# Performance work log

Measured on AMD Instinct MI355X. Metric: run time of the kernel, lower is better.

## Reference

```python
import jax, jax.numpy as jnp
import numpy as np

T, N = 64, 128          # temporal / spatial graph sizes; M = T*N product-graph nodes
B, F_IN, HID, F_OUT = 2, 32, 32, 16
L, K = 2, 4             # num_layers, filter order


def _sym_norm(key, n):
    # random symmetric adjacency, then D^{-1/2} A D^{-1/2} / 2 as in the torch __init__
    a = jax.random.uniform(key, (n, n), dtype=jnp.float32)
    a = 0.5 * (a + a.T)
    d = jnp.sum(a, axis=1)
    dinv = 1.0 / jnp.sqrt(d)
    return (dinv[:, None] * a * dinv[None, :]) * 0.5


def setup_inputs() -> dict:
    key = jax.random.key(0)
    ks = jax.random.split(key, 9)
    x = jax.random.normal(ks[0], (B, T * N, F_IN), dtype=jnp.float32)
    Adj_t = _sym_norm(ks[1], T)
    Adj_s = _sym_norm(ks[2], N)
    s = jax.random.normal(ks[3], (4,), dtype=jnp.float32) * 0.25
    H = jax.random.normal(ks[4], (L, K, HID, HID), dtype=jnp.float32) * 0.1
    W1 = jax.random.normal(ks[5], (F_IN, HID), dtype=jnp.float32) * (1.0 / np.sqrt(F_IN))
    b1 = jax.random.normal(ks[6], (HID,), dtype=jnp.float32) * 0.01
    W2 = jax.random.normal(ks[7], (HID, F_OUT), dtype=jnp.float32) * (1.0 / np.sqrt(HID))
    b2 = jax.random.normal(ks[8], (F_OUT,), dtype=jnp.float32) * 0.01
    return {"x": x, "Adj_t": Adj_t, "Adj_s": Adj_s, "s": s, "H": H,
            "W1": W1, "b1": b1, "W2": W2, "b2": b2}


def reference(x, Adj_t, Adj_s, s, H, W1, b1, W2, b2):
    t, n = Adj_t.shape[0], Adj_s.shape[0]
    I_t = jnp.eye(t, dtype=jnp.float32)
    I_s = jnp.eye(n, dtype=jnp.float32)
    # Adj = s0*I + s1*kron(I_t, Adj_s) + s2*kron(Adj_t, I_s) + s3*kron(Adj_t, Adj_s)
    Adj = (s[0] * jnp.eye(t * n, dtype=jnp.float32)
           + s[1] * jnp.kron(I_t, Adj_s)
           + s[2] * jnp.kron(Adj_t, I_s)
           + s[3] * jnp.kron(Adj_t, Adj_s))
    h = x @ W1 + b1                                   # [B, M, HID]
    num_layers = H.shape[0]
    for l in range(num_layers):
        Ah = jnp.einsum('mn,bnh->bmh', Adj, h)        # Adj @ x, hoisted out of k-loop
        # sum_k (Adj@x) @ H[l,k]  ==  einsum over k and h simultaneously
        h = jnp.tanh(jnp.einsum('bmh,khf->bmf', Ah, H[l]))
    return h @ W2 + b2                                # [B, M, F_OUT]
```

## Files before the change

kernel.cpp:

```cpp
#include <hip/hip_runtime.h>

#define T_DIM 64
#define N_DIM 128
#define BATCH 2
#define HIDW  32


__device__ __forceinline__ int rfl(int x) { return __builtin_amdgcn_readfirstlane(x); }

template<bool PROJ>
__global__ __launch_bounds__(512) void k_temporal(
    const float* __restrict__ src,
    const float* __restrict__ At,
    const float* __restrict__ W1, const float* __restrict__ b1,
    const float* __restrict__ s,
    const float* __restrict__ H, float* __restrict__ Hsum_ws,
    float* __restrict__ up, float* __restrict__ pp)
{
    __shared__ float At_s[64 * 68];
    __shared__ float xs[64 * 36];
    __shared__ float h_loc[64 * 36];

    const int tid = threadIdx.x;
    const int b   = blockIdx.x >> 7;
    const int n   = blockIdx.x & 127;
    const int fg  = tid >> 6;
    const int t   = tid & 63;
    const int fg4u = rfl(fg * 4);

    const float s0v = s[0], s1v = s[1], s2v = s[2], s3v = s[3];

    if (PROJ && blockIdx.x < 4) {
        int idx = blockIdx.x * 512 + tid;
        int l = idx >> 10, rem = idx & 1023;
        const float* Hl = H + l * 4096;
        Hsum_ws[idx] = Hl[rem] + Hl[1024 + rem] + Hl[2048 + rem] + Hl[3072 + rem];
    }

#pragma unroll
    for (int i = 0; i < 8; ++i) {
        int p = tid + 512 * i;
        At_s[(p >> 6) * 68 + (p & 63)] = At[p];
    }

    float h0, h1, h2, h3;
    if (PROJ) {
        {
            int tt = tid >> 3, c4 = tid & 7;
            float4 v = *(const float4*)(src + ((size_t)(b * 8192 + tt * 128 + n)) * 32 + c4 * 4);
            *(float4*)&xs[tt * 36 + c4 * 4] = v;
        }
        __syncthreads();
        const float* W1u = W1 + fg4u;
        float4 bv = *(const float4*)(b1 + fg4u);
        h0 = bv.x; h1 = bv.y; h2 = bv.z; h3 = bv.w;
#pragma unroll
        for (int k4 = 0; k4 < 8; ++k4) {
            float4 xv = *(const float4*)&xs[t * 36 + k4 * 4];
            float4 w0 = *(const float4*)(W1u + (k4 * 4 + 0) * 32);
            float4 w1 = *(const float4*)(W1u + (k4 * 4 + 1) * 32);
            float4 w2 = *(const float4*)(W1u + (k4 * 4 + 2) * 32);
            float4 w3 = *(const float4*)(W1u + (k4 * 4 + 3) * 32);
            h0 += xv.x * w0.x + xv.y * w1.x + xv.z * w2.x + xv.w * w3.x;
            h1 += xv.x * w0.y + xv.y * w1.y + xv.z * w2.y + xv.w * w3.y;
            h2 += xv.x * w0.z + xv.y * w1.z + xv.z * w2.z + xv.w * w3.z;
            h3 += xv.x * w0.w + xv.y * w1.w + xv.z * w2.w + xv.w * w3.w;
        }
        float4 hv; hv.x = h0; hv.y = h1; hv.z = h2; hv.w = h3;
        *(float4*)&h_loc[t * 36 + fg * 4] = hv;
        __syncthreads();
    } else {
        __syncthreads();
        float4 hv = *(const float4*)(src + (((size_t)(b * 128 + n)) * 64 + t) * 32 + fg * 4);
        h0 = hv.x; h1 = hv.y; h2 = hv.z; h3 = hv.w;
    }

    float w0 = 0.f, w1 = 0.f, w2 = 0.f, w3 = 0.f;
    const float* hrow = PROJ ? nullptr
                             : (src + rfl((b * 128 + n) * 2048) + fg4u);
#pragma unroll
    for (int u4 = 0; u4 < 16; ++u4) {
        float4 av = *(const float4*)&At_s[t * 68 + u4 * 4];
        float4 g0, g1, g2, g3;
        if (PROJ) {
            g0 = *(const float4*)&h_loc[(u4 * 4 + 0) * 36 + fg * 4];
            g1 = *(const float4*)&h_loc[(u4 * 4 + 1) * 36 + fg * 4];
            g2 = *(const float4*)&h_loc[(u4 * 4 + 2) * 36 + fg * 4];
            g3 = *(const float4*)&h_loc[(u4 * 4 + 3) * 36 + fg * 4];
        } else {
            g0 = *(const float4*)(hrow + (u4 * 4 + 0) * 32);
            g1 = *(const float4*)(hrow + (u4 * 4 + 1) * 32);
            g2 = *(const float4*)(hrow + (u4 * 4 + 2) * 32);
            g3 = *(const float4*)(hrow + (u4 * 4 + 3) * 32);
        }
        w0 += av.x * g0.x + av.y * g1.x + av.z * g2.x + av.w * g3.x;
        w1 += av.x * g0.y + av.y * g1.y + av.z * g2.y + av.w * g3.y;
        w2 += av.x * g0.z + av.y * g1.z + av.z * g2.z + av.w * g3.z;
        w3 += av.x * g0.w + av.y * g1.w + av.z * g2.w + av.w * g3.w;
    }
    float4 u4v, p4v;
    u4v.x = s1v * h0 + s3v * w0;  p4v.x = s0v * h0 + s2v * w0;
    u4v.y = s1v * h1 + s3v * w1;  p4v.y = s0v * h1 + s2v * w1;
    u4v.z = s1v * h2 + s3v * w2;  p4v.z = s0v * h2 + s2v * w2;
    u4v.w = s1v * h3 + s3v * w3;  p4v.w = s0v * h3 + s2v * w3;
    size_t base = ((size_t)((b * 64 + t) * 128 + n)) * 32 + fg * 4;
    *(float4*)(up + base) = u4v;
    *(float4*)(pp + base) = p4v;
}

template<bool LAST>
__global__ __launch_bounds__(512) void k_spatial(
    const float* __restrict__ up, const float* __restrict__ pp,
    const float* __restrict__ As, const float* __restrict__ Hsum_ws, int layer,
    const float* __restrict__ W2, const float* __restrict__ b2,
    float* __restrict__ hout, float* __restrict__ out)
{
    __shared__ float As_s[64 * 132];
    __shared__ float Ah_s[64 * 36];
    __shared__ float T_s[64 * 36];

    const int tid = threadIdx.x;
    const int b   = blockIdx.x >> 7;
    const int t   = (blockIdx.x >> 1) & 63;
    const int mh  = blockIdx.x & 1;
    const int fg  = tid >> 6;
    const int m   = tid & 63;
    const int fg4u = rfl(fg * 4);

#pragma unroll
    for (int i = 0; i < 4; ++i) {
        int p = tid + 512 * i;
        int r = p >> 5, g = p & 31;
        float4 v = *(const float4*)(As + ((size_t)(mh * 64 + r)) * 128 + g * 4);
        *(float4*)&As_s[r * 132 + g * 4] = v;
    }
    float4 pv = *(const float4*)(pp + (((size_t)(b * 64 + t)) * 128 + mh * 64 + m) * 32 + fg * 4);
    float a0 = pv.x, a1 = pv.y, a2 = pv.z, a3 = pv.w;
    __syncthreads();

    const float* urow = up + rfl((b * 64 + t) * 4096) + fg4u;
#pragma unroll 8
    for (int n4 = 0; n4 < 32; ++n4) {
        float4 av = *(const float4*)&As_s[m * 132 + n4 * 4];
        float4 u0 = *(const float4*)(urow + (n4 * 4 + 0) * 32);
        float4 u1 = *(const float4*)(urow + (n4 * 4 + 1) * 32);
        float4 u2 = *(const float4*)(urow + (n4 * 4 + 2) * 32);
        float4 u3 = *(const float4*)(urow + (n4 * 4 + 3) * 32);
        a0 += av.x * u0.x + av.y * u1.x + av.z * u2.x + av.w * u3.x;
        a1 += av.x * u0.y + av.y * u1.y + av.z * u2.y + av.w * u3.y;
        a2 += av.x * u0.z + av.y * u1.z + av.z * u2.z + av.w * u3.z;
        a3 += av.x * u0.w + av.y * u1.w + av.z * u2.w + av.w * u3.w;
    }
    {
        float4 w; w.x = a0; w.y = a1; w.z = a2; w.w = a3;
        *(float4*)&Ah_s[m * 36 + fg * 4] = w;
    }
    __syncthreads();

    const float* hsrow = Hsum_ws + rfl(layer * 1024) + fg4u;
    float c0 = 0.f, c1 = 0.f, c2 = 0.f, c3 = 0.f;
#pragma unroll
    for (int k4 = 0; k4 < 8; ++k4) {
        float4 av = *(const float4*)&Ah_s[m * 36 + k4 * 4];
        float4 q0 = *(const float4*)(hsrow + (k4 * 4 + 0) * 32);
        float4 q1 = *(const float4*)(hsrow + (k4 * 4 + 1) * 32);
        float4 q2 = *(const float4*)(hsrow + (k4 * 4 + 2) * 32);
        float4 q3 = *(const float4*)(hsrow + (k4 * 4 + 3) * 32);
        c0 += av.x * q0.x + av.y * q1.x + av.z * q2.x + av.w * q3.x;
        c1 += av.x * q0.y + av.y * q1.y + av.z * q2.y + av.w * q3.y;
        c2 += av.x * q0.z + av.y * q1.z + av.z * q2.z + av.w * q3.z;
        c3 += av.x * q0.w + av.y * q1.w + av.z * q2.w + av.w * q3.w;
    }
    c0 = tanhf(c0); c1 = tanhf(c1); c2 = tanhf(c2); c3 = tanhf(c3);

    if (!LAST) {
        float4 o; o.x = c0; o.y = c1; o.z = c2; o.w = c3;
        *(float4*)(hout + (((size_t)(b * 128 + mh * 64 + m)) * 64 + t) * 32 + fg * 4) = o;
    } else {
        float4 w; w.x = c0; w.y = c1; w.z = c2; w.w = c3;
        *(float4*)&T_s[m * 36 + fg * 4] = w;
        __syncthreads();
        const int fg2u = rfl(fg * 2);
        float o0 = b2[fg2u], o1 = b2[fg2u + 1];
        const float* w2r = W2 + fg2u;
#pragma unroll
        for (int k4 = 0; k4 < 8; ++k4) {
            float4 tv = *(const float4*)&T_s[m * 36 + k4 * 4];
            float2 v0 = *(const float2*)(w2r + (k4 * 4 + 0) * 16);
            float2 v1 = *(const float2*)(w2r + (k4 * 4 + 1) * 16);
            float2 v2 = *(const float2*)(w2r + (k4 * 4 + 2) * 16);
            float2 v3 = *(const float2*)(w2r + (k4 * 4 + 3) * 16);
            o0 += tv.x * v0.x + tv.y * v1.x + tv.z * v2.x + tv.w * v3.x;
            o1 += tv.x * v0.y + tv.y * v1.y + tv.z * v2.y + tv.w * v3.y;
        }
        float2 o; o.x = o0; o.y = o1;
        *(float2*)(out + (((size_t)(b * 64 + t)) * 128 + mh * 64 + m) * 16 + fg * 2) = o;
    }
}

extern "C" void kernel_launch(void* const* d_in, const int* in_sizes, int n_in,
                              void* d_out, int out_size, void* d_ws, size_t ws_size,
                              hipStream_t stream)
{
    const float* x   = (const float*)d_in[0];
    const float* At  = (const float*)d_in[1];
    const float* As  = (const float*)d_in[2];
    const float* s   = (const float*)d_in[3];
    const float* H   = (const float*)d_in[4];
    const float* W1  = (const float*)d_in[5];
    const float* b1  = (const float*)d_in[6];
    const float* W2  = (const float*)d_in[7];
    const float* b2  = (const float*)d_in[8];
    float* out = (float*)d_out;

    float* up   = (float*)d_ws;
    float* pp   = up + 524288;
    float* h    = pp + 524288;
    float* Hsum = h  + 524288;

    k_temporal<true ><<<256, 512, 0, stream>>>(x, At, W1, b1, s, H, Hsum, up, pp);
    k_spatial <false><<<256, 512, 0, stream>>>(up, pp, As, Hsum, 0, W2, b2, h, out);
    k_temporal<false><<<256, 512, 0, stream>>>(h, At, W1, b1, s, H, Hsum, up, pp);
    k_spatial <true ><<<256, 512, 0, stream>>>(up, pp, As, Hsum, 1, W2, b2, h, out);
}
```

Baseline: 40.13 us.

## Stage operands in XOR-swizzled shared memory and compute H sums per block

Replaces padded shared-memory layouts with an XOR swizzle and stages more operands in LDS. W1, W2, the spatial up-row and the temporal h-tile now go to shared memory instead of being read from global memory inside the inner loops. The per-layer sum of H over k is now computed redundantly in every spatial block rather than in a few blocks of the first kernel, which removes the Hsum workspace. The intent is cheaper, conflict-free LDS reads in place of repeated global loads, at the cost of higher LDS use per block (which may lower occupancy) and duplicated H summation.

```diff
diff --git a/kernel.cpp b/kernel.cpp
--- a/kernel.cpp
+++ b/kernel.cpp
@@ -1,12 +1,7 @@
 #include <hip/hip_runtime.h>
 
-#define T_DIM 64
-#define N_DIM 128
-#define BATCH 2
-#define HIDW  32
-
-
-__device__ __forceinline__ int rfl(int x) { return __builtin_amdgcn_readfirstlane(x); }
+
+__device__ __forceinline__ int swz(int row, int g) { return g ^ (row & 7); }
 
 template<bool PROJ>
 __global__ __launch_bounds__(512) void k_temporal(
@@ -14,110 +9,99 @@
     const float* __restrict__ At,
     const float* __restrict__ W1, const float* __restrict__ b1,
     const float* __restrict__ s,
-    const float* __restrict__ H, float* __restrict__ Hsum_ws,
     float* __restrict__ up, float* __restrict__ pp)
 {
-    __shared__ float At_s[64 * 68];
-    __shared__ float xs[64 * 36];
-    __shared__ float h_loc[64 * 36];
+    __shared__ float At_s[64 * 64];
+    __shared__ float xs  [64 * 32];
+    __shared__ float hls [64 * 32];
+    __shared__ float W1s [1024];
 
     const int tid = threadIdx.x;
     const int b   = blockIdx.x >> 7;
     const int n   = blockIdx.x & 127;
     const int fg  = tid >> 6;
-    const int t   = tid & 63;
-    const int fg4u = rfl(fg * 4);
+    const int lt  = tid & 63;
 
     const float s0v = s[0], s1v = s[1], s2v = s[2], s3v = s[3];
-
-    if (PROJ && blockIdx.x < 4) {
-        int idx = blockIdx.x * 512 + tid;
-        int l = idx >> 10, rem = idx & 1023;
-        const float* Hl = H + l * 4096;
-        Hsum_ws[idx] = Hl[rem] + Hl[1024 + rem] + Hl[2048 + rem] + Hl[3072 + rem];
-    }
 
 #pragma unroll
     for (int i = 0; i < 8; ++i) {
         int p = tid + 512 * i;
-        At_s[(p >> 6) * 68 + (p & 63)] = At[p];
-    }
-
-    float h0, h1, h2, h3;
+        int r = p >> 6, c = p & 63;
+        At_s[r * 64 + (swz(r, c >> 2) << 2) + (c & 3)] = At[p];
+    }
+
     if (PROJ) {
         {
             int tt = tid >> 3, c4 = tid & 7;
             float4 v = *(const float4*)(src + ((size_t)(b * 8192 + tt * 128 + n)) * 32 + c4 * 4);
-            *(float4*)&xs[tt * 36 + c4 * 4] = v;
-        }
-        __syncthreads();
-        const float* W1u = W1 + fg4u;
-        float4 bv = *(const float4*)(b1 + fg4u);
-        h0 = bv.x; h1 = bv.y; h2 = bv.z; h3 = bv.w;
+            *(float4*)&xs[tt * 32 + (swz(tt, c4) << 2)] = v;
+        }
+        if (tid < 256) ((float4*)W1s)[tid] = ((const float4*)W1)[tid];
+        __syncthreads();
+        float4 bv = *(const float4*)(b1 + fg * 4);
+        float h0 = bv.x, h1 = bv.y, h2 = bv.z, h3 = bv.w;
 #pragma unroll
         for (int k4 = 0; k4 < 8; ++k4) {
-            float4 xv = *(const float4*)&xs[t * 36 + k4 * 4];
-            float4 w0 = *(const float4*)(W1u + (k4 * 4 + 0) * 32);
-            float4 w1 = *(const float4*)(W1u + (k4 * 4 + 1) * 32);
-            float4 w2 = *(const float4*)(W1u + (k4 * 4 + 2) * 32);
-            float4 w3 = *(const float4*)(W1u + (k4 * 4 + 3) * 32);
+            float4 xv = *(const float4*)&xs[lt * 32 + (swz(lt, k4) << 2)];
+            float4 w0 = *(const float4*)&W1s[(k4 * 4 + 0) * 32 + fg * 4];
+            float4 w1 = *(const float4*)&W1s[(k4 * 4 + 1) * 32 + fg * 4];
+            float4 w2 = *(const float4*)&W1s[(k4 * 4 + 2) * 32 + fg * 4];
+            float4 w3 = *(const float4*)&W1s[(k4 * 4 + 3) * 32 + fg * 4];
             h0 += xv.x * w0.x + xv.y * w1.x + xv.z * w2.x + xv.w * w3.x;
             h1 += xv.x * w0.y + xv.y * w1.y + xv.z * w2.y + xv.w * w3.y;
             h2 += xv.x * w0.z + xv.y * w1.z + xv.z * w2.z + xv.w * w3.z;
             h3 += xv.x * w0.w + xv.y * w1.w + xv.z * w2.w + xv.w * w3.w;
         }
         float4 hv; hv.x = h0; hv.y = h1; hv.z = h2; hv.w = h3;
-        *(float4*)&h_loc[t * 36 + fg * 4] = hv;
+        *(float4*)&hls[lt * 32 + (swz(lt, fg) << 2)] = hv;
         __syncthreads();
     } else {
-        __syncthreads();
-        float4 hv = *(const float4*)(src + (((size_t)(b * 128 + n)) * 64 + t) * 32 + fg * 4);
-        h0 = hv.x; h1 = hv.y; h2 = hv.z; h3 = hv.w;
-    }
-
+        {
+            int tt = tid >> 3, c4 = tid & 7;
+            float4 v = *(const float4*)(src + ((size_t)(b * 128 + n)) * 2048 + tt * 32 + c4 * 4);
+            *(float4*)&hls[tt * 32 + (swz(tt, c4) << 2)] = v;
+        }
+        __syncthreads();
+    }
+
+    float4 hv = *(const float4*)&hls[lt * 32 + (swz(lt, fg) << 2)];
     float w0 = 0.f, w1 = 0.f, w2 = 0.f, w3 = 0.f;
-    const float* hrow = PROJ ? nullptr
-                             : (src + rfl((b * 128 + n) * 2048) + fg4u);
 #pragma unroll
     for (int u4 = 0; u4 < 16; ++u4) {
-        float4 av = *(const float4*)&At_s[t * 68 + u4 * 4];
-        float4 g0, g1, g2, g3;
-        if (PROJ) {
-            g0 = *(const float4*)&h_loc[(u4 * 4 + 0) * 36 + fg * 4];
-            g1 = *(const float4*)&h_loc[(u4 * 4 + 1) * 36 + fg * 4];
-            g2 = *(const float4*)&h_loc[(u4 * 4 + 2) * 36 + fg * 4];
-            g3 = *(const float4*)&h_loc[(u4 * 4 + 3) * 36 + fg * 4];
-        } else {
-            g0 = *(const float4*)(hrow + (u4 * 4 + 0) * 32);
-            g1 = *(const float4*)(hrow + (u4 * 4 + 1) * 32);
-            g2 = *(const float4*)(hrow + (u4 * 4 + 2) * 32);
-            g3 = *(const float4*)(hrow + (u4 * 4 + 3) * 32);
-        }
+        float4 av = *(const float4*)&At_s[lt * 64 + (swz(lt, u4) << 2)];
+        float4 g0 = *(const float4*)&hls[(u4 * 4 + 0) * 32 + (swz(u4 * 4 + 0, fg) << 2)];
+        float4 g1 = *(const float4*)&hls[(u4 * 4 + 1) * 32 + (swz(u4 * 4 + 1, fg) << 2)];
+        float4 g2 = *(const float4*)&hls[(u4 * 4 + 2) * 32 + (swz(u4 * 4 + 2, fg) << 2)];
+        float4 g3 = *(const float4*)&hls[(u4 * 4 + 3) * 32 + (swz(u4 * 4 + 3, fg) << 2)];
         w0 += av.x * g0.x + av.y * g1.x + av.z * g2.x + av.w * g3.x;
         w1 += av.x * g0.y + av.y * g1.y + av.z * g2.y + av.w * g3.y;
         w2 += av.x * g0.z + av.y * g1.z + av.z * g2.z + av.w * g3.z;
         w3 += av.x * g0.w + av.y * g1.w + av.z * g2.w + av.w * g3.w;
     }
-    float4 u4v, p4v;
-    u4v.x = s1v * h0 + s3v * w0;  p4v.x = s0v * h0 + s2v * w0;
-    u4v.y = s1v * h1 + s3v * w1;  p4v.y = s0v * h1 + s2v * w1;
-    u4v.z = s1v * h2 + s3v * w2;  p4v.z = s0v * h2 + s2v * w2;
-    u4v.w = s1v * h3 + s3v * w3;  p4v.w = s0v * h3 + s2v * w3;
-    size_t base = ((size_t)((b * 64 + t) * 128 + n)) * 32 + fg * 4;
-    *(float4*)(up + base) = u4v;
-    *(float4*)(pp + base) = p4v;
+    float4 uo, po;
+    uo.x = s1v * hv.x + s3v * w0;  po.x = s0v * hv.x + s2v * w0;
+    uo.y = s1v * hv.y + s3v * w1;  po.y = s0v * hv.y + s2v * w1;
+    uo.z = s1v * hv.z + s3v * w2;  po.z = s0v * hv.z + s2v * w2;
+    uo.w = s1v * hv.w + s3v * w3;  po.w = s0v * hv.w + s2v * w3;
+    size_t base = ((size_t)((b * 64 + lt) * 128 + n)) * 32 + fg * 4;
+    *(float4*)(up + base) = uo;
+    *(float4*)(pp + base) = po;
 }
 
 template<bool LAST>
 __global__ __launch_bounds__(512) void k_spatial(
     const float* __restrict__ up, const float* __restrict__ pp,
-    const float* __restrict__ As, const float* __restrict__ Hsum_ws, int layer,
+    const float* __restrict__ As, const float* __restrict__ H, int layer,
     const float* __restrict__ W2, const float* __restrict__ b2,
     float* __restrict__ hout, float* __restrict__ out)
 {
-    __shared__ float As_s[64 * 132];
-    __shared__ float Ah_s[64 * 36];
-    __shared__ float T_s[64 * 36];
+    __shared__ float As_s[64 * 128];
+    __shared__ float up_s[128 * 32];
+    __shared__ float Ah_s[64 * 32];
+    __shared__ float T_s [64 * 32];
+    __shared__ float Hs  [1024];
+    __shared__ float W2s [512];
 
     const int tid = threadIdx.x;
     const int b   = blockIdx.x >> 7;
@@ -125,47 +109,58 @@
     const int mh  = blockIdx.x & 1;
     const int fg  = tid >> 6;
     const int m   = tid & 63;
-    const int fg4u = rfl(fg * 4);
 
 #pragma unroll
     for (int i = 0; i < 4; ++i) {
         int p = tid + 512 * i;
         int r = p >> 5, g = p & 31;
         float4 v = *(const float4*)(As + ((size_t)(mh * 64 + r)) * 128 + g * 4);
-        *(float4*)&As_s[r * 132 + g * 4] = v;
-    }
-    float4 pv = *(const float4*)(pp + (((size_t)(b * 64 + t)) * 128 + mh * 64 + m) * 32 + fg * 4);
+        *(float4*)&As_s[r * 128 + (swz(r, g) << 2)] = v;
+    }
+    {
+        const float* usrc = up + ((size_t)(b * 64 + t)) * 4096;
+        ((float4*)up_s)[tid]       = ((const float4*)usrc)[tid];
+        ((float4*)up_s)[tid + 512] = ((const float4*)usrc)[tid + 512];
+    }
+    {
+        const float* Hl = H + layer * 4096;
+#pragma unroll
+        for (int i = 0; i < 2; ++i) {
+            int p = tid + 512 * i;
+            Hs[p] = Hl[p] + Hl[1024 + p] + Hl[2048 + p] + Hl[3072 + p];
+        }
+    }
+    if (LAST && tid < 128) ((float4*)W2s)[tid] = ((const float4*)W2)[tid];
+    float4 pv = *(const float4*)(pp + ((size_t)((b * 64 + t) * 128 + mh * 64 + m)) * 32 + fg * 4);
     float a0 = pv.x, a1 = pv.y, a2 = pv.z, a3 = pv.w;
     __syncthreads();
 
-    const float* urow = up + rfl((b * 64 + t) * 4096) + fg4u;
 #pragma unroll 8
     for (int n4 = 0; n4 < 32; ++n4) {
-        float4 av = *(const float4*)&As_s[m * 132 + n4 * 4];
-        float4 u0 = *(const float4*)(urow + (n4 * 4 + 0) * 32);
-        float4 u1 = *(const float4*)(urow + (n4 * 4 + 1) * 32);
-        float4 u2 = *(const float4*)(urow + (n4 * 4 + 2) * 32);
-        float4 u3 = *(const float4*)(urow + (n4 * 4 + 3) * 32);
+        float4 av = *(const float4*)&As_s[m * 128 + (swz(m, n4) << 2)];
+        float4 u0 = *(const float4*)&up_s[(n4 * 4 + 0) * 32 + fg * 4];
+        float4 u1 = *(const float4*)&up_s[(n4 * 4 + 1) * 32 + fg * 4];
+        float4 u2 = *(const float4*)&up_s[(n4 * 4 + 2) * 32 + fg * 4];
+        float4 u3 = *(const float4*)&up_s[(n4 * 4 + 3) * 32 + fg * 4];
         a0 += av.x * u0.x + av.y * u1.x + av.z * u2.x + av.w * u3.x;
         a1 += av.x * u0.y + av.y * u1.y + av.z * u2.y + av.w * u3.y;
         a2 += av.x * u0.z + av.y * u1.z + av.z * u2.z + av.w * u3.z;
         a3 += av.x * u0.w + av.y * u1.w + av.z * u2.w + av.w * u3.w;
     }
     {
-        float4 w; w.x = a0; w.y = a1; w.z = a2; w.w = a3;
-        *(float4*)&Ah_s[m * 36 + fg * 4] = w;
+        float4 t4; t4.x = a0; t4.y = a1; t4.z = a2; t4.w = a3;
+        *(float4*)&Ah_s[m * 32 + (swz(m, fg) << 2)] = t4;
     }
     __syncthreads();
 
-    const float* hsrow = Hsum_ws + rfl(layer * 1024) + fg4u;
     float c0 = 0.f, c1 = 0.f, c2 = 0.f, c3 = 0.f;
 #pragma unroll
     for (int k4 = 0; k4 < 8; ++k4) {
-        float4 av = *(const float4*)&Ah_s[m * 36 + k4 * 4];
-        float4 q0 = *(const float4*)(hsrow + (k4 * 4 + 0) * 32);
-        float4 q1 = *(const float4*)(hsrow + (k4 * 4 + 1) * 32);
-        float4 q2 = *(const float4*)(hsrow + (k4 * 4 + 2) * 32);
-        float4 q3 = *(const float4*)(hsrow + (k4 * 4 + 3) * 32);
+        float4 av = *(const float4*)&Ah_s[m * 32 + (swz(m, k4) << 2)];
+        float4 q0 = *(const float4*)&Hs[(k4 * 4 + 0) * 32 + fg * 4];
+        float4 q1 = *(const float4*)&Hs[(k4 * 4 + 1) * 32 + fg * 4];
+        float4 q2 = *(const float4*)&Hs[(k4 * 4 + 2) * 32 + fg * 4];
+        float4 q3 = *(const float4*)&Hs[(k4 * 4 + 3) * 32 + fg * 4];
         c0 += av.x * q0.x + av.y * q1.x + av.z * q2.x + av.w * q3.x;
         c1 += av.x * q0.y + av.y * q1.y + av.z * q2.y + av.w * q3.y;
         c2 += av.x * q0.z + av.y * q1.z + av.z * q2.z + av.w * q3.z;
@@ -177,24 +172,23 @@
         float4 o; o.x = c0; o.y = c1; o.z = c2; o.w = c3;
         *(float4*)(hout + (((size_t)(b * 128 + mh * 64 + m)) * 64 + t) * 32 + fg * 4) = o;
     } else {
-        float4 w; w.x = c0; w.y = c1; w.z = c2; w.w = c3;
-        *(float4*)&T_s[m * 36 + fg * 4] = w;
-        __syncthreads();
-        const int fg2u = rfl(fg * 2);
-        float o0 = b2[fg2u], o1 = b2[fg2u + 1];
-        const float* w2r = W2 + fg2u;
+        float4 t4; t4.x = c0; t4.y = c1; t4.z = c2; t4.w = c3;
+        *(float4*)&T_s[m * 32 + (swz(m, fg) << 2)] = t4;
+        __syncthreads();
+        const int fo = fg * 2;
+        float o0 = b2[fo], o1 = b2[fo + 1];
 #pragma unroll
         for (int k4 = 0; k4 < 8; ++k4) {
-            float4 tv = *(const float4*)&T_s[m * 36 + k4 * 4];
-            float2 v0 = *(const float2*)(w2r + (k4 * 4 + 0) * 16);
-            float2 v1 = *(const float2*)(w2r + (k4 * 4 + 1) * 16);
-            float2 v2 = *(const float2*)(w2r + (k4 * 4 + 2) * 16);
-            float2 v3 = *(const float2*)(w2r + (k4 * 4 + 3) * 16);
+            float4 tv = *(const float4*)&T_s[m * 32 + (swz(m, k4) << 2)];
+            float2 v0 = *(const float2*)&W2s[(k4 * 4 + 0) * 16 + fo];
+            float2 v1 = *(const float2*)&W2s[(k4 * 4 + 1) * 16 + fo];
+            float2 v2 = *(const float2*)&W2s[(k4 * 4 + 2) * 16 + fo];
+            float2 v3 = *(const float2*)&W2s[(k4 * 4 + 3) * 16 + fo];
             o0 += tv.x * v0.x + tv.y * v1.x + tv.z * v2.x + tv.w * v3.x;
             o1 += tv.x * v0.y + tv.y * v1.y + tv.z * v2.y + tv.w * v3.y;
         }
-        float2 o; o.x = o0; o.y = o1;
-        *(float2*)(out + (((size_t)(b * 64 + t)) * 128 + mh * 64 + m) * 16 + fg * 2) = o;
+        float2 o2; o2.x = o0; o2.y = o1;
+        *(float2*)(out + ((size_t)((b * 64 + t) * 128 + mh * 64 + m)) * 16 + fo) = o2;
     }
 }
 
@@ -215,11 +209,10 @@
 
     float* up   = (float*)d_ws;
     float* pp   = up + 524288;
-    float* h    = pp + 524288;
-    float* Hsum = h  + 524288;
-
-    k_temporal<true ><<<256, 512, 0, stream>>>(x, At, W1, b1, s, H, Hsum, up, pp);
-    k_spatial <false><<<256, 512, 0, stream>>>(up, pp, As, Hsum, 0, W2, b2, h, out);
-    k_temporal<false><<<256, 512, 0, stream>>>(h, At, W1, b1, s, H, Hsum, up, pp);
-    k_spatial <true ><<<256, 512, 0, stream>>>(up, pp, As, Hsum, 1, W2, b2, h, out);
+    float* hbuf = pp + 524288;
+
+    k_temporal<true ><<<256, 512, 0, stream>>>(x,    At, W1, b1, s, up, pp);
+    k_spatial <false><<<256, 512, 0, stream>>>(up, pp, As, H, 0, W2, b2, hbuf, out);
+    k_temporal<false><<<256, 512, 0, stream>>>(hbuf, At, W1, b1, s, up, pp);
+    k_spatial <true ><<<256, 512, 0, stream>>>(up, pp, As, H, 1, W2, b2, hbuf, out);
 }
```

Result: faster. 32.77 us, median of 2 (-18.3%).
